# Optimization experiments

Hardware: AMD Instinct MI355X
Metric: run time of the kernel (lower is better)

The kernel has to match this reference:

```python
import jax, jax.numpy as jnp
import numpy as np

# PyG RGATConv defaults: attention_mechanism='across-relation',
# attention_mode='additive-self-attention', dim=1, negative_slope=0.2.
# Dropout is a no-op in eval mode (reference is deterministic).
HEADS = 8
OUT = 64          # hidden_size (per-head out_channels)
R = 8             # num_relations
NEG_SLOPE = 0.2


def segment_softmax(logits, seg, num_segments):
    # PyG softmax: stable per-destination-node softmax with +1e-16 in denom
    m = jax.ops.segment_max(logits, seg, num_segments=num_segments)
    ex = jnp.exp(logits - m[seg])
    s = jax.ops.segment_sum(ex, seg, num_segments=num_segments)
    return ex / (s[seg] + 1e-16)


def rgat_layer(x, src, dst, etype, eattr, W, q, k, We, e, bias, concat, num_nodes):
    # W: [R, F_in, HEADS*OUT]. Transform all nodes under every relation once,
    # then gather per edge -- same math as x_j @ W[edge_type] but avoids the
    # huge [E, F_in, H*OUT] per-edge weight gather.
    t = jnp.einsum('nf,rfh->rnh', x, W)           # [R, N, H*OUT]
    qn = t @ q                                    # [R, N, HEADS] (dim=1)
    kn = t @ k                                    # [R, N, HEADS]
    qi = qn[etype, dst]                           # [E, HEADS]
    kj = kn[etype, src]                           # [E, HEADS]
    ae = (eattr @ We) @ e                         # [E, HEADS] edge-attr fusion
    alpha = jax.nn.leaky_relu(qi + kj + ae, NEG_SLOPE)
    alpha = segment_softmax(alpha, dst, num_nodes)           # across-relation softmax
    out_j = t[etype, src].reshape(-1, HEADS, OUT)            # [E, H, OUT]
    agg = jax.ops.segment_sum(alpha[:, :, None] * out_j, dst,
                              num_segments=num_nodes)        # [N, H, OUT]
    out = agg.reshape(num_nodes, HEADS * OUT) if concat else agg.mean(axis=1)
    return out + bias


def setup_inputs() -> dict:
    key = jax.random.key(0)
    ks = jax.random.split(key, 16)
    N, E, F = 16000, 256000, 256
    H = HEADS * OUT  # 512

    def p(k, shape, fan_in):
        return jax.random.normal(k, shape, jnp.float32) * np.float32(1.0 / np.sqrt(fan_in))

    return dict(
        x=jax.random.normal(ks[0], (N, F), jnp.float32),
        edge_index=jax.random.randint(ks[1], (2, E), 0, N, dtype=jnp.int32),
        edge_type=jax.random.randint(ks[2], (E,), 0, R, dtype=jnp.int32),
        edge_attr=jax.random.uniform(ks[3], (E, 1), jnp.float32),
        W1=p(ks[4], (R, F, H), F), q1=p(ks[5], (H, HEADS), H), k1=p(ks[6], (H, HEADS), H),
        We1=p(ks[7], (1, H), 1), e1=p(ks[8], (H, HEADS), H), b1=jnp.zeros((H,), jnp.float32),
        W2=p(ks[9], (R, H, H), H), q2=p(ks[10], (H, HEADS), H), k2=p(ks[11], (H, HEADS), H),
        We2=p(ks[12], (1, H), 1), e2=p(ks[13], (H, HEADS), H), b2=jnp.zeros((OUT,), jnp.float32),
    )


def reference(x, edge_index, edge_type, edge_attr,
              W1, q1, k1, We1, e1, b1,
              W2, q2, k2, We2, e2, b2):
    N = x.shape[0]
    # add_self_loops with edge_attr fill_value=0.5
    loop = jnp.arange(N, dtype=edge_index.dtype)
    src = jnp.concatenate([edge_index[0], loop])
    dst = jnp.concatenate([edge_index[1], loop])
    ea = jnp.concatenate([edge_attr, jnp.full((N, edge_attr.shape[1]), 0.5, edge_attr.dtype)])
    # self-loop edge type = (max(edge_type)+1) % num_relations
    slt = jnp.mod(edge_type.max() + 1, R).astype(edge_type.dtype)
    et = jnp.concatenate([edge_type, jnp.full((N,), 1, edge_type.dtype) * slt])

    h = rgat_layer(x, src, dst, et, ea, W1, q1, k1, We1, e1, b1, True, N)    # [N, H*OUT]
    out = rgat_layer(h, src, dst, et, ea, W2, q2, k2, We2, e2, b2, False, N)  # [N, OUT]
    return out
```

## Files before the change

kernel.cpp:

```cpp
#include <hip/hip_runtime.h>
#include <hip/hip_bf16.h>
#include <cstdint>
#include <cstddef>

#define NN 16000
#define MPAD 16128
#define EE 256000
#define ETOT (EE + NN)
#define RREL 8
#define NHEAD 8
#define DOUT 64
#define HD 512
#define NEG 0.2f
#define NMAIN 1008

typedef unsigned int u32;
typedef short bf16x8 __attribute__((ext_vector_type(8)));
typedef float f32x4 __attribute__((ext_vector_type(4)));

__device__ inline unsigned short f2bf(float f) {
  u32 i = __float_as_uint(f);
  u32 r = (i + 0x7fff + ((i >> 16) & 1)) >> 16;
  return (unsigned short)r;
}
__device__ inline float bf2f(unsigned short h) {
  return __uint_as_float((u32)h << 16);
}
__device__ inline void g2lds16(const void* g, void* lds) {
  __builtin_amdgcn_global_load_lds(
      (const __attribute__((address_space(1))) unsigned int*)g,
      (__attribute__((address_space(3))) unsigned int*)lds, 16, 0, 0);
}

__global__ void k_hist(const int* __restrict__ ei, const int* __restrict__ et,
                       int* __restrict__ deg, int* __restrict__ meta) {
  int e = blockIdx.x * 256 + threadIdx.x;
  if (e >= ETOT) return;
  int dst;
  if (e < EE) { dst = ei[EE + e]; atomicMax(&meta[0], et[e]); }
  else dst = e - EE;
  atomicAdd(&deg[dst], 1);
}

__global__ __launch_bounds__(1024) void k_scan(const int* __restrict__ deg,
                                               int* __restrict__ rowptr,
                                               int* __restrict__ fill) {
  __shared__ int sm[1024];
  const int tid = threadIdx.x;
  const int base = tid * 16;
  int local[16];
  int s = 0;
#pragma unroll
  for (int i = 0; i < 16; ++i) {
    int idx = base + i;
    int v = (idx < NN) ? deg[idx] : 0;
    local[i] = s;
    s += v;
  }
  sm[tid] = s;
  __syncthreads();
  for (int off = 1; off < 1024; off <<= 1) {
    int t = (tid >= off) ? sm[tid - off] : 0;
    __syncthreads();
    sm[tid] += t;
    __syncthreads();
  }
  const int pre = (tid > 0) ? sm[tid - 1] : 0;
#pragma unroll
  for (int i = 0; i < 16; ++i) {
    int idx = base + i;
    if (idx < NN) { rowptr[idx] = pre + local[i]; fill[idx] = pre + local[i]; }
  }
  if (tid == 1023) rowptr[NN] = sm[1023];
}

__global__ void k_scatter(const int* __restrict__ ei, const int* __restrict__ et,
                          const float* __restrict__ ea, const int* __restrict__ meta,
                          int* __restrict__ fill, int* __restrict__ csr_src,
                          int* __restrict__ csr_et, float* __restrict__ csr_ea) {
  int e = blockIdx.x * 256 + threadIdx.x;
  if (e >= ETOT) return;
  int src, dst, r; float a;
  if (e < EE) { src = ei[e]; dst = ei[EE + e]; r = et[e]; a = ea[e]; }
  else { src = dst = e - EE; r = (meta[0] + 1) & (RREL - 1); a = 0.5f; }
  int pos = atomicAdd(&fill[dst], 1);
  csr_src[pos] = src; csr_et[pos] = r; csr_ea[pos] = a;
}

__global__ void k_wqk(const float* __restrict__ W, const float* __restrict__ q,
                      const float* __restrict__ k, const float* __restrict__ We,
                      const float* __restrict__ e, unsigned short* __restrict__ WQKT,
                      float* __restrict__ cvec, int F) {
  if ((int)blockIdx.x == (RREL * F * 16) / 256) {
    int j = threadIdx.x;
    if (j < NHEAD) {
      float acc = 0.f;
      for (int h2 = 0; h2 < HD; ++h2) acc += We[h2] * e[h2 * NHEAD + j];
      cvec[j] = acc;
    }
    return;
  }
  int g = blockIdx.x * 256 + threadIdx.x;
  int j = g & 15;
  int rf = g >> 4;
  int f = rf % F;
  const float* wrow = W + (size_t)rf * HD;
  const float* qk = ((j < 8) ? q : k) + (j & 7);
  float acc = 0.f;
  for (int h = 0; h < HD; ++h) acc += wrow[h] * qk[(size_t)h * NHEAD];
  const int col = (rf / F) * 16 + j;
  WQKT[(size_t)col * F + f] = f2bf(acc);
}

__global__ void k_asplit(const float* __restrict__ in, unsigned short* __restrict__ A2,
                         int F) {
  long idx = (long)blockIdx.x * 256 + threadIdx.x;
  long total = (long)NN * (F >> 2);
  if (idx >= total) return;
  int row = (int)(idx / (F >> 2));
  int c4 = (int)(idx % (F >> 2)) << 2;
  float4 v = *(const float4*)&in[(size_t)row * F + c4];
  ushort4 hi;
  hi.x = f2bf(v.x); hi.y = f2bf(v.y); hi.z = f2bf(v.z); hi.w = f2bf(v.w);
  *(ushort4*)&A2[(size_t)row * F + c4] = hi;
}

__global__ __launch_bounds__(256) void k_bsplit(const float* __restrict__ W,
                                                unsigned short* __restrict__ BT, int F) {
  int f0 = blockIdx.x * 64, c0 = blockIdx.y * 64, r = blockIdx.z;
  __shared__ float tile[64][65];
  int tid = threadIdx.x;
  int i0 = tid >> 6;
  int j = tid & 63;
  const float* Wr = W + (size_t)r * F * 512;
  for (int i = i0; i < 64; i += 4)
    tile[i][j] = Wr[(size_t)(f0 + i) * 512 + c0 + j];
  __syncthreads();
  unsigned short* Br = BT + (size_t)r * 512 * F;
  for (int c = i0; c < 64; c += 4) {
    float v = tile[j][c];
    Br[(size_t)(c0 + c) * F + f0 + j] = f2bf(v);
  }
}

__global__ __launch_bounds__(512, 2) void k_mgemm(const unsigned short* __restrict__ A2,
                                                  const unsigned short* __restrict__ BT,
                                                  const unsigned short* __restrict__ WQKT,
                                                  unsigned short* __restrict__ Ct,
                                                  float* __restrict__ qkbuf,
                                                  int Kp) {
  const int bid = blockIdx.x;
  const bool isqk = (bid >= NMAIN);
  int m0, n0;
  const unsigned short* Bbase;
  if (!isqk) {
    const int v = (bid & 7) * 126 + (bid >> 3);
    m0 = (v >> 4) << 8;
    n0 = (v & 15) << 8;
    Bbase = BT;
  } else {
    m0 = (bid - NMAIN) << 8;
    n0 = 0;
    Bbase = WQKT;
  }

  __shared__ __align__(16) unsigned short smem[49152];

  const int tid = threadIdx.x;
  const int wid = tid >> 6;
  const int lane = tid & 63;
  const int wr = wid >> 2;
  const int wc = wid & 3;
  const int rlow = lane & 15;
  const int kch = lane >> 4;

  const unsigned short* srcA[2];
  const unsigned short* srcB[2];
  int dstOff[2];
#pragma unroll
  for (int p = 0; p < 2; ++p) {
    int fr = (p << 3) + wid;
    srcA[p] = A2 + (size_t)(m0 + fr * 16 + rlow) * Kp + kch * 8;
    srcB[p] = Bbase + (size_t)(n0 + fr * 16 + rlow) * Kp + kch * 8;
    dstOff[p] = fr * 512;
  }

  f32x4 acc[8][4] = {};
  const int nt = Kp >> 5;

#pragma unroll
  for (int tp = 0; tp < 2; ++tp) {
    const int ko = tp << 5;
#pragma unroll
    for (int p = 0; p < 2; ++p) {
      g2lds16(srcA[p] + ko, &smem[tp * 8192 + dstOff[p]]);
      g2lds16(srcB[p] + ko, &smem[24576 + tp * 8192 + dstOff[p]]);
    }
  }

  int buf = 0;
  for (int u = 0; u < nt; ++u) {
    if (u + 1 < nt)
      asm volatile("s_waitcnt vmcnt(4)" ::: "memory");
    else
      asm volatile("s_waitcnt vmcnt(0)" ::: "memory");
    __builtin_amdgcn_s_barrier();
    asm volatile("" ::: "memory");
    if (u + 2 < nt) {
      int nb2 = buf + 2; if (nb2 >= 3) nb2 -= 3;
      const int ko = (u + 2) << 5;
#pragma unroll
      for (int p = 0; p < 2; ++p) {
        g2lds16(srcA[p] + ko, &smem[nb2 * 8192 + dstOff[p]]);
        g2lds16(srcB[p] + ko, &smem[24576 + nb2 * 8192 + dstOff[p]]);
      }
    }
    const unsigned short* Ab = smem + buf * 8192;
    const unsigned short* Bb = smem + 24576 + buf * 8192;
    bf16x8 af[8], bv[4];
#pragma unroll
    for (int i = 0; i < 8; ++i)
      af[i] = *(const bf16x8*)&Ab[(wr * 8 + i) * 512 + lane * 8];
#pragma unroll
    for (int j = 0; j < 4; ++j)
      bv[j] = *(const bf16x8*)&Bb[(wc * 4 + j) * 512 + lane * 8];
    __builtin_amdgcn_s_setprio(1);
#pragma unroll
    for (int i = 0; i < 8; ++i)
#pragma unroll
      for (int j = 0; j < 4; ++j)
        acc[i][j] = __builtin_amdgcn_mfma_f32_16x16x32_bf16(af[i], bv[j],
                                                            acc[i][j], 0, 0, 0);
    __builtin_amdgcn_s_setprio(0);
    buf = (buf == 2) ? 0 : buf + 1;
  }

  if (!isqk) {
    __syncthreads();
    float* epsW = (float*)smem + wid * 1344;
    const int rowL = lane & 15;
    const int cseg = lane >> 4;
    const int colfull0 = n0 + wc * 64;
    const int rr = colfull0 >> 9;
    const int hbase = (colfull0 & 511) + cseg * 16;
#pragma unroll
    for (int i = 0; i < 8; ++i) {
#pragma unroll
      for (int j = 0; j < 4; ++j)
        *(f32x4*)&epsW[(j * 16 + rlow) * 21 + kch * 4] = acc[i][j];
      float vals[16];
#pragma unroll
      for (int c = 0; c < 16; ++c) vals[c] = epsW[(cseg * 16 + c) * 21 + rowL];
      const int rowg = m0 + wr * 128 + i * 16 + rowL;
      unsigned short* dst = Ct + ((size_t)rr * MPAD + rowg) * HD + hbase;
      uint4 w0, w1;
      w0.x = (u32)f2bf(vals[0])  | ((u32)f2bf(vals[1])  << 16);
      w0.y = (u32)f2bf(vals[2])  | ((u32)f2bf(vals[3])  << 16);
      w0.z = (u32)f2bf(vals[4])  | ((u32)f2bf(vals[5])  << 16);
      w0.w = (u32)f2bf(vals[6])  | ((u32)f2bf(vals[7])  << 16);
      w1.x = (u32)f2bf(vals[8])  | ((u32)f2bf(vals[9])  << 16);
      w1.y = (u32)f2bf(vals[10]) | ((u32)f2bf(vals[11]) << 16);
      w1.z = (u32)f2bf(vals[12]) | ((u32)f2bf(vals[13]) << 16);
      w1.w = (u32)f2bf(vals[14]) | ((u32)f2bf(vals[15]) << 16);
      *(uint4*)dst = w0;
      *(uint4*)(dst + 8) = w1;
    }
  } else {
    if (wc < 2) {
#pragma unroll
      for (int i = 0; i < 8; ++i) {
        const int row0 = m0 + wr * 128 + i * 16 + kch * 4;
#pragma unroll
        for (int j = 0; j < 4; ++j) {
          const int col = wc * 64 + j * 16 + rlow;
#pragma unroll
          for (int q = 0; q < 4; ++q) {
            const int row = row0 + q;
            if (row < NN) qkbuf[(size_t)row * 128 + col] = acc[i][j][q];
          }
        }
      }
    }
  }
}

template <int CONCAT>
__global__ __launch_bounds__(256) void k_attn(const unsigned short* __restrict__ t,
    const float* __restrict__ qkbuf, const float* __restrict__ cvec,
    const int* __restrict__ rowptr, const int* __restrict__ csr_src,
    const int* __restrict__ csr_et, const float* __restrict__ csr_ea,
    const float* __restrict__ bias, float* __restrict__ out,
    unsigned short* __restrict__ A2out) {
  const int wv = threadIdx.x >> 6;
  const int lane = threadIdx.x & 63;
  const int n = blockIdx.x * 4 + wv;
  const int h = lane >> 3;
  const int c0 = lane << 3;
  const int e0 = rowptr[n], e1 = rowptr[n + 1];
  const float ch = cvec[h];
  const float* qrow = qkbuf + (size_t)n * 128;
  float m = -1e30f, l = 0.f;
  float acc[8] = {};
  int rN = csr_et[e0];
  float aN = csr_ea[e0];
  int sN = csr_src[e0];
  uint4 tvN = *(const uint4*)&t[((size_t)rN * MPAD + sN) * HD + c0];
  float klogN = qkbuf[(size_t)sN * 128 + rN * 16 + 8 + h];
  for (int e = e0; e < e1; ++e) {
    const int r = rN;
    const float a = aN;
    const uint4 tv = tvN;
    const float klog = klogN;
    const float qv = qrow[r * 16 + h];
    if (e + 1 < e1) {
      const int s2 = csr_src[e + 1];
      rN = csr_et[e + 1];
      aN = csr_ea[e + 1];
      tvN = *(const uint4*)&t[((size_t)rN * MPAD + s2) * HD + c0];
      klogN = qkbuf[(size_t)s2 * 128 + rN * 16 + 8 + h];
    }
    float logit = qv + klog + a * ch;
    logit = (logit > 0.f) ? logit : NEG * logit;
    float p;
    if (logit <= m) {
      p = __expf(logit - m);
    } else {
      const float sc = __expf(m - logit);
      l *= sc;
#pragma unroll
      for (int c = 0; c < 8; ++c) acc[c] *= sc;
      m = logit;
      p = 1.f;
    }
    l += p;
    acc[0] = fmaf(p, __uint_as_float((tv.x & 0xffffu) << 16), acc[0]);
    acc[1] = fmaf(p, __uint_as_float(tv.x & 0xffff0000u), acc[1]);
    acc[2] = fmaf(p, __uint_as_float((tv.y & 0xffffu) << 16), acc[2]);
    acc[3] = fmaf(p, __uint_as_float(tv.y & 0xffff0000u), acc[3]);
    acc[4] = fmaf(p, __uint_as_float((tv.z & 0xffffu) << 16), acc[4]);
    acc[5] = fmaf(p, __uint_as_float(tv.z & 0xffff0000u), acc[5]);
    acc[6] = fmaf(p, __uint_as_float((tv.w & 0xffffu) << 16), acc[6]);
    acc[7] = fmaf(p, __uint_as_float(tv.w & 0xffff0000u), acc[7]);
  }
  const float inv = 1.f / (l + 1e-16f);
  if (CONCAT) {
    unsigned short his[8];
#pragma unroll
    for (int c = 0; c < 8; ++c)
      his[c] = f2bf(fmaf(acc[c], inv, bias[c0 + c]));
    uint4 wh;
    wh.x = (u32)his[0] | ((u32)his[1] << 16);
    wh.y = (u32)his[2] | ((u32)his[3] << 16);
    wh.z = (u32)his[4] | ((u32)his[5] << 16);
    wh.w = (u32)his[6] | ((u32)his[7] << 16);
    *(uint4*)&A2out[(size_t)n * 512 + c0] = wh;
  } else {
    __shared__ float sm[4][HD];
#pragma unroll
    for (int c = 0; c < 8; ++c) sm[wv][c0 + c] = acc[c] * inv;
    __syncthreads();
    const int d = lane;
    float s = 0.f;
#pragma unroll
    for (int hh = 0; hh < NHEAD; ++hh) s += sm[wv][hh * 64 + d];
    out[(size_t)n * DOUT + d] = s * 0.125f + bias[d];
  }
}

static void run_pipeline(const float* x, const int* ei, const int* et, const float* ea,
                         const float* W1, const float* q1, const float* k1,
                         const float* We1, const float* e1, const float* b1,
                         const float* W2, const float* q2, const float* k2,
                         const float* We2, const float* e2, const float* b2,
                         float* out, float* qkbuf, unsigned short* WQKT,
                         unsigned short* A2, unsigned short* BT,
                         float* cvec, int* meta, int* deg, int* rowptr,
                         int* fill, int* csr_src, int* csr_et, float* csr_ea,
                         unsigned short* t, hipStream_t stream) {
  (void)hipMemsetAsync(meta, 0, 4, stream);
  (void)hipMemsetAsync(deg, 0, (size_t)NN * 4, stream);
  k_hist<<<(ETOT + 255) / 256, 256, 0, stream>>>(ei, et, deg, meta);
  k_scan<<<1, 1024, 0, stream>>>(deg, rowptr, fill);
  k_scatter<<<(ETOT + 255) / 256, 256, 0, stream>>>(ei, et, ea, meta, fill,
                                                    csr_src, csr_et, csr_ea);
  k_wqk<<<RREL * 256 * 16 / 256 + 1, 256, 0, stream>>>(W1, q1, k1, We1, e1, WQKT,
                                                       cvec, 256);
  k_asplit<<<(NN * 64 + 255) / 256, 256, 0, stream>>>(x, A2, 256);
  k_bsplit<<<dim3(4, 8, RREL), 256, 0, stream>>>(W1, BT, 256);
  k_mgemm<<<NMAIN + 63, 512, 0, stream>>>(A2, BT, WQKT, t, qkbuf, 256);
  k_attn<1><<<NN / 4, 256, 0, stream>>>(t, qkbuf, cvec, rowptr, csr_src, csr_et,
                                        csr_ea, b1, nullptr, A2);
  k_wqk<<<RREL * HD * 16 / 256 + 1, 256, 0, stream>>>(W2, q2, k2, We2, e2, WQKT,
                                                      cvec, HD);
  k_bsplit<<<dim3(8, 8, RREL), 256, 0, stream>>>(W2, BT, HD);
  k_mgemm<<<NMAIN + 63, 512, 0, stream>>>(A2, BT, WQKT, t, qkbuf, 512);
  k_attn<0><<<NN / 4, 256, 0, stream>>>(t, qkbuf, cvec, rowptr, csr_src, csr_et,
                                        csr_ea, b2, out, nullptr);
}

extern "C" void kernel_launch(void* const* d_in, const int* in_sizes, int n_in,
                              void* d_out, int out_size, void* d_ws, size_t ws_size,
                              hipStream_t stream) {
  const float* x   = (const float*)d_in[0];
  const int*   ei  = (const int*)d_in[1];
  const int*   et  = (const int*)d_in[2];
  const float* ea  = (const float*)d_in[3];
  const float* W1  = (const float*)d_in[4];
  const float* q1  = (const float*)d_in[5];
  const float* k1  = (const float*)d_in[6];
  const float* We1 = (const float*)d_in[7];
  const float* e1  = (const float*)d_in[8];
  const float* b1  = (const float*)d_in[9];
  const float* W2  = (const float*)d_in[10];
  const float* q2  = (const float*)d_in[11];
  const float* k2  = (const float*)d_in[12];
  const float* We2 = (const float*)d_in[13];
  const float* e2  = (const float*)d_in[14];
  const float* b2  = (const float*)d_in[15];
  float* out = (float*)d_out;

  char* w = (char*)d_ws;
  auto alloc = [&](size_t bytes) {
    char* p = w;
    w += (bytes + 255) & ~(size_t)255;
    return p;
  };
  float* qkbuf  = (float*)alloc((size_t)NN * 128 * 4);
  unsigned short* WQKT = (unsigned short*)alloc((size_t)256 * HD * 2);
  unsigned short* A2 = (unsigned short*)alloc((size_t)MPAD * HD * 2);
  unsigned short* BT = (unsigned short*)alloc((size_t)RREL * HD * HD * 2);
  float* cvec   = (float*)alloc(64);
  int*   meta   = (int*)alloc(64);
  int*   deg    = (int*)alloc((size_t)NN * 4);
  int*   rowptr = (int*)alloc((size_t)(NN + 1) * 4);
  int*   fill   = (int*)alloc((size_t)NN * 4);
  int*   csr_src= (int*)alloc((size_t)ETOT * 4);
  int*   csr_et = (int*)alloc((size_t)ETOT * 4);
  float* csr_ea = (float*)alloc((size_t)ETOT * 4);
  unsigned short* t = (unsigned short*)alloc((size_t)RREL * MPAD * HD * 2);
  (void)ws_size;

  run_pipeline(x, ei, et, ea, W1, q1, k1, We1, e1, b1,
               W2, q2, k2, We2, e2, b2, out, qkbuf, WQKT, A2, BT,
               cvec, meta, deg, rowptr, fill, csr_src, csr_et, csr_ea,
               t, stream);
}
```

Measured before the change: 476.4 us.

## Merge independent prep kernels and overlap layer-2 weight prep with layer-1 attention

```diff
diff --git a/kernel.cpp b/kernel.cpp
--- a/kernel.cpp
+++ b/kernel.cpp
@@ -13,6 +13,13 @@
 #define HD 512
 #define NEG 0.2f
 #define NMAIN 1008
+#define NBH 1063
+#define NBA 4000
+#define NBW1 129
+#define NBB1 256
+#define NBATT 4000
+#define NBB2 512
+#define NBW2 257
 
 typedef unsigned int u32;
 typedef short bf16x8 __attribute__((ext_vector_type(8)));
@@ -32,14 +39,182 @@
       (__attribute__((address_space(3))) unsigned int*)lds, 16, 0, 0);
 }
 
-__global__ void k_hist(const int* __restrict__ ei, const int* __restrict__ et,
-                       int* __restrict__ deg, int* __restrict__ meta) {
-  int e = blockIdx.x * 256 + threadIdx.x;
+__device__ __forceinline__ void dev_hist(int bid, const int* __restrict__ ei,
+                                         const int* __restrict__ et,
+                                         int* __restrict__ deg, int* meta) {
+  int e = bid * 256 + (int)threadIdx.x;
   if (e >= ETOT) return;
   int dst;
   if (e < EE) { dst = ei[EE + e]; atomicMax(&meta[0], et[e]); }
   else dst = e - EE;
   atomicAdd(&deg[dst], 1);
+}
+
+__device__ __forceinline__ void dev_asplit(int bid, const float* __restrict__ in,
+                                           unsigned short* __restrict__ A2, int F) {
+  long idx = (long)bid * 256 + threadIdx.x;
+  long total = (long)NN * (F >> 2);
+  if (idx >= total) return;
+  int row = (int)(idx / (F >> 2));
+  int c4 = (int)(idx % (F >> 2)) << 2;
+  float4 v = *(const float4*)&in[(size_t)row * F + c4];
+  ushort4 hi;
+  hi.x = f2bf(v.x); hi.y = f2bf(v.y); hi.z = f2bf(v.z); hi.w = f2bf(v.w);
+  *(ushort4*)&A2[(size_t)row * F + c4] = hi;
+}
+
+__device__ __forceinline__ void dev_wqk(int bid, int nmain, const float* __restrict__ W,
+                                        const float* __restrict__ q,
+                                        const float* __restrict__ k,
+                                        const float* __restrict__ We,
+                                        const float* __restrict__ e,
+                                        unsigned short* __restrict__ WQKT,
+                                        float* __restrict__ cvec, int F) {
+  if (bid == nmain) {
+    int j = threadIdx.x;
+    if (j < NHEAD) {
+      float acc = 0.f;
+      for (int h2 = 0; h2 < HD; ++h2) acc += We[h2] * e[h2 * NHEAD + j];
+      cvec[j] = acc;
+    }
+    return;
+  }
+  int g = bid * 256 + (int)threadIdx.x;
+  int j = g & 15;
+  int rf = g >> 4;
+  int f = rf % F;
+  const float* wrow = W + (size_t)rf * HD;
+  const float* qk = ((j < 8) ? q : k) + (j & 7);
+  float acc = 0.f;
+  for (int h = 0; h < HD; ++h) acc += wrow[h] * qk[(size_t)h * NHEAD];
+  const int col = (rf / F) * 16 + j;
+  WQKT[(size_t)col * F + f] = f2bf(acc);
+}
+
+__device__ void dev_bsplit(int f0b, int c0b, int r, const float* __restrict__ W,
+                           unsigned short* __restrict__ BT, int F,
+                           float (*tile)[65]) {
+  const int f0 = f0b * 64, c0 = c0b * 64;
+  int tid = threadIdx.x;
+  int i0 = tid >> 6;
+  int j = tid & 63;
+  const float* Wr = W + (size_t)r * F * 512;
+  for (int i = i0; i < 64; i += 4)
+    tile[i][j] = Wr[(size_t)(f0 + i) * 512 + c0 + j];
+  __syncthreads();
+  unsigned short* Br = BT + (size_t)r * 512 * F;
+  for (int c = i0; c < 64; c += 4) {
+    float v = tile[j][c];
+    Br[(size_t)(c0 + c) * F + f0 + j] = f2bf(v);
+  }
+}
+
+__device__ __forceinline__ void dev_attn1(int bid, const unsigned short* __restrict__ t,
+    const float* __restrict__ qkbuf, const float* __restrict__ cvec,
+    const int* __restrict__ rowptr, const int* __restrict__ csr_src,
+    const int* __restrict__ csr_et, const float* __restrict__ csr_ea,
+    const float* __restrict__ bias, unsigned short* __restrict__ A2out) {
+  const int wv = threadIdx.x >> 6;
+  const int lane = threadIdx.x & 63;
+  const int n = bid * 4 + wv;
+  const int h = lane >> 3;
+  const int c0 = lane << 3;
+  const int e0 = rowptr[n], e1 = rowptr[n + 1];
+  const float ch = cvec[h];
+  const float* qrow = qkbuf + (size_t)n * 128;
+  float m = -1e30f, l = 0.f;
+  float acc[8] = {};
+  int rN = csr_et[e0];
+  float aN = csr_ea[e0];
+  int sN = csr_src[e0];
+  uint4 tvN = *(const uint4*)&t[((size_t)rN * MPAD + sN) * HD + c0];
+  float klogN = qkbuf[(size_t)sN * 128 + rN * 16 + 8 + h];
+  for (int e = e0; e < e1; ++e) {
+    const int r = rN;
+    const float a = aN;
+    const uint4 tv = tvN;
+    const float klog = klogN;
+    const float qv = qrow[r * 16 + h];
+    if (e + 1 < e1) {
+      const int s2 = csr_src[e + 1];
+      rN = csr_et[e + 1];
+      aN = csr_ea[e + 1];
+      tvN = *(const uint4*)&t[((size_t)rN * MPAD + s2) * HD + c0];
+      klogN = qkbuf[(size_t)s2 * 128 + rN * 16 + 8 + h];
+    }
+    float logit = qv + klog + a * ch;
+    logit = (logit > 0.f) ? logit : NEG * logit;
+    float p;
+    if (logit <= m) {
+      p = __expf(logit - m);
+    } else {
+      const float sc = __expf(m - logit);
+      l *= sc;
+#pragma unroll
+      for (int c = 0; c < 8; ++c) acc[c] *= sc;
+      m = logit;
+      p = 1.f;
+    }
+    l += p;
+    acc[0] = fmaf(p, __uint_as_float((tv.x & 0xffffu) << 16), acc[0]);
+    acc[1] = fmaf(p, __uint_as_float(tv.x & 0xffff0000u), acc[1]);
+    acc[2] = fmaf(p, __uint_as_float((tv.y & 0xffffu) << 16), acc[2]);
+    acc[3] = fmaf(p, __uint_as_float(tv.y & 0xffff0000u), acc[3]);
+    acc[4] = fmaf(p, __uint_as_float((tv.z & 0xffffu) << 16), acc[4]);
+    acc[5] = fmaf(p, __uint_as_float(tv.z & 0xffff0000u), acc[5]);
+    acc[6] = fmaf(p, __uint_as_float((tv.w & 0xffffu) << 16), acc[6]);
+    acc[7] = fmaf(p, __uint_as_float(tv.w & 0xffff0000u), acc[7]);
+  }
+  const float inv = 1.f / (l + 1e-16f);
+  unsigned short his[8];
+#pragma unroll
+  for (int c = 0; c < 8; ++c)
+    his[c] = f2bf(fmaf(acc[c], inv, bias[c0 + c]));
+  uint4 wh;
+  wh.x = (u32)his[0] | ((u32)his[1] << 16);
+  wh.y = (u32)his[2] | ((u32)his[3] << 16);
+  wh.z = (u32)his[4] | ((u32)his[5] << 16);
+  wh.w = (u32)his[6] | ((u32)his[7] << 16);
+  *(uint4*)&A2out[(size_t)n * 512 + c0] = wh;
+}
+
+__global__ __launch_bounds__(256) void k_prep1(const int* __restrict__ ei,
+    const int* __restrict__ et, int* __restrict__ deg, int* meta,
+    const float* __restrict__ x, unsigned short* __restrict__ A2,
+    const float* __restrict__ W1, const float* __restrict__ q1,
+    const float* __restrict__ k1, const float* __restrict__ We1,
+    const float* __restrict__ e1, unsigned short* __restrict__ WQKT,
+    float* __restrict__ cvec1, unsigned short* __restrict__ BT) {
+  __shared__ float tile[64][65];
+  int b = blockIdx.x;
+  if (b < NBH) { dev_hist(b, ei, et, deg, meta); return; }
+  b -= NBH;
+  if (b < NBA) { dev_asplit(b, x, A2, 256); return; }
+  b -= NBA;
+  if (b < NBW1) { dev_wqk(b, NBW1 - 1, W1, q1, k1, We1, e1, WQKT, cvec1, 256); return; }
+  b -= NBW1;
+  dev_bsplit(b & 3, (b >> 2) & 7, b >> 5, W1, BT, 256, tile);
+}
+
+__global__ __launch_bounds__(256) void k_attn1f(const unsigned short* __restrict__ t,
+    const float* __restrict__ qkbuf, const float* __restrict__ cvec1,
+    const int* __restrict__ rowptr, const int* __restrict__ csr_src,
+    const int* __restrict__ csr_et, const float* __restrict__ csr_ea,
+    const float* __restrict__ b1, unsigned short* __restrict__ A2out,
+    const float* __restrict__ W2, const float* __restrict__ q2,
+    const float* __restrict__ k2, const float* __restrict__ We2,
+    const float* __restrict__ e2, unsigned short* __restrict__ WQKT,
+    float* __restrict__ cvec2, unsigned short* __restrict__ BT) {
+  __shared__ float tile[64][65];
+  int b = blockIdx.x;
+  if (b < NBATT) {
+    dev_attn1(b, t, qkbuf, cvec1, rowptr, csr_src, csr_et, csr_ea, b1, A2out);
+    return;
+  }
+  b -= NBATT;
+  if (b < NBB2) { dev_bsplit(b & 7, (b >> 3) & 7, b >> 6, W2, BT, 512, tile); return; }
+  b -= NBB2;
+  dev_wqk(b, NBW2 - 1, W2, q2, k2, We2, e2, WQKT, cvec2, 512);
 }
 
 __global__ __launch_bounds__(1024) void k_scan(const int* __restrict__ deg,
@@ -85,62 +260,6 @@
   else { src = dst = e - EE; r = (meta[0] + 1) & (RREL - 1); a = 0.5f; }
   int pos = atomicAdd(&fill[dst], 1);
   csr_src[pos] = src; csr_et[pos] = r; csr_ea[pos] = a;
-}
-
-__global__ void k_wqk(const float* __restrict__ W, const float* __restrict__ q,
-                      const float* __restrict__ k, const float* __restrict__ We,
-                      const float* __restrict__ e, unsigned short* __restrict__ WQKT,
-                      float* __restrict__ cvec, int F) {
-  if ((int)blockIdx.x == (RREL * F * 16) / 256) {
-    int j = threadIdx.x;
-    if (j < NHEAD) {
-      float acc = 0.f;
-      for (int h2 = 0; h2 < HD; ++h2) acc += We[h2] * e[h2 * NHEAD + j];
-      cvec[j] = acc;
-    }
-    return;
-  }
-  int g = blockIdx.x * 256 + threadIdx.x;
-  int j = g & 15;
-  int rf = g >> 4;
-  int f = rf % F;
-  const float* wrow = W + (size_t)rf * HD;
-  const float* qk = ((j < 8) ? q : k) + (j & 7);
-  float acc = 0.f;
-  for (int h = 0; h < HD; ++h) acc += wrow[h] * qk[(size_t)h * NHEAD];
-  const int col = (rf / F) * 16 + j;
-  WQKT[(size_t)col * F + f] = f2bf(acc);
-}
-
-__global__ void k_asplit(const float* __restrict__ in, unsigned short* __restrict__ A2,
-                         int F) {
-  long idx = (long)blockIdx.x * 256 + threadIdx.x;
-  long total = (long)NN * (F >> 2);
-  if (idx >= total) return;
-  int row = (int)(idx / (F >> 2));
-  int c4 = (int)(idx % (F >> 2)) << 2;
-  float4 v = *(const float4*)&in[(size_t)row * F + c4];
-  ushort4 hi;
-  hi.x = f2bf(v.x); hi.y = f2bf(v.y); hi.z = f2bf(v.z); hi.w = f2bf(v.w);
-  *(ushort4*)&A2[(size_t)row * F + c4] = hi;
-}
-
-__global__ __launch_bounds__(256) void k_bsplit(const float* __restrict__ W,
-                                                unsigned short* __restrict__ BT, int F) {
-  int f0 = blockIdx.x * 64, c0 = blockIdx.y * 64, r = blockIdx.z;
-  __shared__ float tile[64][65];
-  int tid = threadIdx.x;
-  int i0 = tid >> 6;
-  int j = tid & 63;
-  const float* Wr = W + (size_t)r * F * 512;
-  for (int i = i0; i < 64; i += 4)
-    tile[i][j] = Wr[(size_t)(f0 + i) * 512 + c0 + j];
-  __syncthreads();
-  unsigned short* Br = BT + (size_t)r * 512 * F;
-  for (int c = i0; c < 64; c += 4) {
-    float v = tile[j][c];
-    Br[(size_t)(c0 + c) * F + f0 + j] = f2bf(v);
-  }
 }
 
 __global__ __launch_bounds__(512, 2) void k_mgemm(const unsigned short* __restrict__ A2,
@@ -284,13 +403,11 @@
   }
 }
 
-template <int CONCAT>
-__global__ __launch_bounds__(256) void k_attn(const unsigned short* __restrict__ t,
+__global__ __launch_bounds__(256) void k_attn0(const unsigned short* __restrict__ t,
     const float* __restrict__ qkbuf, const float* __restrict__ cvec,
     const int* __restrict__ rowptr, const int* __restrict__ csr_src,
     const int* __restrict__ csr_et, const float* __restrict__ csr_ea,
-    const float* __restrict__ bias, float* __restrict__ out,
-    unsigned short* __restrict__ A2out) {
+    const float* __restrict__ bias, float* __restrict__ out) {
   const int wv = threadIdx.x >> 6;
   const int lane = threadIdx.x & 63;
   const int n = blockIdx.x * 4 + wv;
@@ -343,59 +460,15 @@
     acc[7] = fmaf(p, __uint_as_float(tv.w & 0xffff0000u), acc[7]);
   }
   const float inv = 1.f / (l + 1e-16f);
-  if (CONCAT) {
-    unsigned short his[8];
-#pragma unroll
-    for (int c = 0; c < 8; ++c)
-      his[c] = f2bf(fmaf(acc[c], inv, bias[c0 + c]));
-    uint4 wh;
-    wh.x = (u32)his[0] | ((u32)his[1] << 16);
-    wh.y = (u32)his[2] | ((u32)his[3] << 16);
-    wh.z = (u32)his[4] | ((u32)his[5] << 16);
-    wh.w = (u32)his[6] | ((u32)his[7] << 16);
-    *(uint4*)&A2out[(size_t)n * 512 + c0] = wh;
-  } else {
-    __shared__ float sm[4][HD];
-#pragma unroll
-    for (int c = 0; c < 8; ++c) sm[wv][c0 + c] = acc[c] * inv;
-    __syncthreads();
-    const int d = lane;
-    float s = 0.f;
-#pragma unroll
-    for (int hh = 0; hh < NHEAD; ++hh) s += sm[wv][hh * 64 + d];
-    out[(size_t)n * DOUT + d] = s * 0.125f + bias[d];
-  }
-}
-
-static void run_pipeline(const float* x, const int* ei, const int* et, const float* ea,
-                         const float* W1, const float* q1, const float* k1,
-                         const float* We1, const float* e1, const float* b1,
-                         const float* W2, const float* q2, const float* k2,
-                         const float* We2, const float* e2, const float* b2,
-                         float* out, float* qkbuf, unsigned short* WQKT,
-                         unsigned short* A2, unsigned short* BT,
-                         float* cvec, int* meta, int* deg, int* rowptr,
-                         int* fill, int* csr_src, int* csr_et, float* csr_ea,
-                         unsigned short* t, hipStream_t stream) {
-  (void)hipMemsetAsync(meta, 0, 4, stream);
-  (void)hipMemsetAsync(deg, 0, (size_t)NN * 4, stream);
-  k_hist<<<(ETOT + 255) / 256, 256, 0, stream>>>(ei, et, deg, meta);
-  k_scan<<<1, 1024, 0, stream>>>(deg, rowptr, fill);
-  k_scatter<<<(ETOT + 255) / 256, 256, 0, stream>>>(ei, et, ea, meta, fill,
-                                                    csr_src, csr_et, csr_ea);
-  k_wqk<<<RREL * 256 * 16 / 256 + 1, 256, 0, stream>>>(W1, q1, k1, We1, e1, WQKT,
-                                                       cvec, 256);
-  k_asplit<<<(NN * 64 + 255) / 256, 256, 0, stream>>>(x, A2, 256);
-  k_bsplit<<<dim3(4, 8, RREL), 256, 0, stream>>>(W1, BT, 256);
-  k_mgemm<<<NMAIN + 63, 512, 0, stream>>>(A2, BT, WQKT, t, qkbuf, 256);
-  k_attn<1><<<NN / 4, 256, 0, stream>>>(t, qkbuf, cvec, rowptr, csr_src, csr_et,
-                                        csr_ea, b1, nullptr, A2);
-  k_wqk<<<RREL * HD * 16 / 256 + 1, 256, 0, stream>>>(W2, q2, k2, We2, e2, WQKT,
-                                                      cvec, HD);
-  k_bsplit<<<dim3(8, 8, RREL), 256, 0, stream>>>(W2, BT, HD);
-  k_mgemm<<<NMAIN + 63, 512, 0, stream>>>(A2, BT, WQKT, t, qkbuf, 512);
-  k_attn<0><<<NN / 4, 256, 0, stream>>>(t, qkbuf, cvec, rowptr, csr_src, csr_et,
-                                        csr_ea, b2, out, nullptr);
+  __shared__ float sm[4][HD];
+#pragma unroll
+  for (int c = 0; c < 8; ++c) sm[wv][c0 + c] = acc[c] * inv;
+  __syncthreads();
+  const int d = lane;
+  float s = 0.f;
+#pragma unroll
+  for (int hh = 0; hh < NHEAD; ++hh) s += sm[wv][hh * 64 + d];
+  out[(size_t)n * DOUT + d] = s * 0.125f + bias[d];
 }
 
 extern "C" void kernel_launch(void* const* d_in, const int* in_sizes, int n_in,
@@ -429,7 +502,8 @@
   unsigned short* WQKT = (unsigned short*)alloc((size_t)256 * HD * 2);
   unsigned short* A2 = (unsigned short*)alloc((size_t)MPAD * HD * 2);
   unsigned short* BT = (unsigned short*)alloc((size_t)RREL * HD * HD * 2);
-  float* cvec   = (float*)alloc(64);
+  float* cvec1  = (float*)alloc(64);
+  float* cvec2  = (float*)alloc(64);
   int*   meta   = (int*)alloc(64);
   int*   deg    = (int*)alloc((size_t)NN * 4);
   int*   rowptr = (int*)alloc((size_t)(NN + 1) * 4);
@@ -440,8 +514,18 @@
   unsigned short* t = (unsigned short*)alloc((size_t)RREL * MPAD * HD * 2);
   (void)ws_size;
 
-  run_pipeline(x, ei, et, ea, W1, q1, k1, We1, e1, b1,
-               W2, q2, k2, We2, e2, b2, out, qkbuf, WQKT, A2, BT,
-               cvec, meta, deg, rowptr, fill, csr_src, csr_et, csr_ea,
-               t, stream);
-}
+  (void)hipMemsetAsync(meta, 0, 4, stream);
+  (void)hipMemsetAsync(deg, 0, (size_t)NN * 4, stream);
+  k_prep1<<<NBH + NBA + NBW1 + NBB1, 256, 0, stream>>>(
+      ei, et, deg, meta, x, A2, W1, q1, k1, We1, e1, WQKT, cvec1, BT);
+  k_scan<<<1, 1024, 0, stream>>>(deg, rowptr, fill);
+  k_scatter<<<(ETOT + 255) / 256, 256, 0, stream>>>(ei, et, ea, meta, fill,
+                                                    csr_src, csr_et, csr_ea);
+  k_mgemm<<<NMAIN + 63, 512, 0, stream>>>(A2, BT, WQKT, t, qkbuf, 256);
+  k_attn1f<<<NBATT + NBB2 + NBW2, 256, 0, stream>>>(
+      t, qkbuf, cvec1, rowptr, csr_src, csr_et, csr_ea, b1, A2,
+      W2, q2, k2, We2, e2, WQKT, cvec2, BT);
+  k_mgemm<<<NMAIN + 63, 512, 0, stream>>>(A2, BT, WQKT, t, qkbuf, 512);
+  k_attn0<<<NN / 4, 256, 0, stream>>>(t, qkbuf, cvec2, rowptr, csr_src, csr_et,
+                                      csr_ea, b2, out);
+}
```

Result: no change. 467.9 us (-1.8%).
